# Performance work log

Measured on AMD Instinct MI355X. Metric: run time of the kernel, lower is better.

Reference implementation:

```python
import jax, jax.numpy as jnp
import numpy as np

N_EXPERTS = 8
D_MODEL = 1024
D_FF = 4096
BATCH = 4
SEQ = 4096


def setup_inputs() -> dict:
    key = jax.random.key(0)
    k1, k2, k3, k4 = jax.random.split(key, 4)
    hidden_states = jax.random.normal(k1, (BATCH, SEQ, D_MODEL), dtype=jnp.float32)
    expert_indices = jax.random.randint(k2, (BATCH, SEQ), 0, N_EXPERTS, dtype=jnp.int64)
    # Expert MLP params, scaled like standard init
    W1 = jax.random.normal(k3, (N_EXPERTS, D_MODEL, D_FF), dtype=jnp.float32) / np.sqrt(D_MODEL)
    b1 = jnp.zeros((N_EXPERTS, D_FF), dtype=jnp.float32)
    W2 = jax.random.normal(k4, (N_EXPERTS, D_FF, D_MODEL), dtype=jnp.float32) / np.sqrt(D_FF)
    b2 = jnp.zeros((N_EXPERTS, D_MODEL), dtype=jnp.float32)
    return {"hidden_states": hidden_states, "expert_indices": expert_indices,
            "W1": W1, "b1": b1, "W2": W2, "b2": b2}


def reference(hidden_states, expert_indices, W1, b1, W2, b2):
    B, S, D = hidden_states.shape
    flat = hidden_states.reshape(B * S, D)          # [T, D]
    idx = expert_indices.reshape(-1)                 # [T]
    out = jnp.zeros_like(flat)
    # Fixed small loop over experts (structurally distinct weights).
    # jit-friendly: each expert runs over all tokens, output masked per token.
    for e in range(W1.shape[0]):
        h = jax.nn.gelu(flat @ W1[e] + b1[e])        # [T, F]
        y = h @ W2[e] + b2[e]                        # [T, D]
        out = out + jnp.where((idx == e)[:, None], y, jnp.float32(0.0))
    return out.reshape(B, S, D)
```

## Files before the change

kernel.cpp:

```cpp
#include <hip/hip_runtime.h>

#define T_TOK 16384
#define DMODEL 1024
#define DFF 4096
#define NEXP 8
#define BM 128
#define BN 128
#define BK 32
#define LDA 40
#define LDB 40
#define TPAD (T_TOK + NEXP * BM)

#define SEG8 256
#define TP256 (T_TOK + NEXP * SEG8)
#define BM2 256
#define BN2 128
#define BK3 32

typedef __bf16 bf16x8 __attribute__((ext_vector_type(8)));
typedef float f32x4 __attribute__((ext_vector_type(4)));

#define GLOAD16(gp, lp) __builtin_amdgcn_global_load_lds( \
    (const __attribute__((address_space(1))) void*)(gp), \
    (__attribute__((address_space(3))) void*)(lp), 16, 0, 0)

#define MFMA16(a, b, c) __builtin_amdgcn_mfma_f32_16x16x32_bf16(a, b, c, 0, 0, 0)

__device__ __forceinline__ float gelu_f(float x) {
  float u = 0.7978845608028654f * (x + 0.044715f * x * x * x);
  float e = __expf(2.0f * u);
  float th = 1.0f - 2.0f / (e + 1.0f);
  return 0.5f * x * (1.0f + th);
}

__global__ void k_init(int* counts, int* cursors, int* bucket, int n) {
  int i = blockIdx.x * blockDim.x + threadIdx.x;
  if (i < n) bucket[i] = -1;
  if (i < NEXP) { counts[i] = 0; cursors[i] = 0; }
}

__global__ void k_hist(const int* __restrict__ idx, int* counts) {
  int t = blockIdx.x * blockDim.x + threadIdx.x;
  int e = (t < T_TOK) ? idx[t] : -1;
#pragma unroll
  for (int ex = 0; ex < NEXP; ex++) {
    unsigned long long m = __ballot(e == ex);
    if (((threadIdx.x & 63) == 0) && m)
      atomicAdd(&counts[ex], __popcll(m));
  }
}

__global__ void k_scan(const int* __restrict__ counts, int* po, int seg) {
  if (threadIdx.x == 0 && blockIdx.x == 0) {
    int acc = 0;
    for (int e = 0; e < NEXP; e++) {
      po[e] = acc;
      acc += ((counts[e] + seg - 1) / seg) * seg;
    }
    po[NEXP] = acc;
  }
}

__global__ void k_scatter(const int* __restrict__ idx, const int* __restrict__ po,
                          int* cursors, int* bucket) {
  int t = blockIdx.x * blockDim.x + threadIdx.x;
  int lane = threadIdx.x & 63;
  int e = (t < T_TOK) ? idx[t] : -1;
#pragma unroll
  for (int ex = 0; ex < NEXP; ex++) {
    unsigned long long m = __ballot(e == ex);
    if (e == ex) {
      int lead = __ffsll((long long)m) - 1;
      unsigned long long before = m & ((lane == 0) ? 0ull : ((1ull << lane) - 1ull));
      int base = 0;
      if (lane == lead) base = atomicAdd(&cursors[ex], __popcll(m));
      base = __shfl(base, lead);
      bucket[po[ex] + base + __popcll(before)] = t;
    }
  }
}

__global__ __launch_bounds__(256) void k_gather(
    const float* __restrict__ X, const int* __restrict__ bucket,
    __bf16* __restrict__ Xg)
{
  const int r = blockIdx.x;
  const int t = bucket[r];
  const int c = threadIdx.x * 4;
  float4 v = {0.f, 0.f, 0.f, 0.f};
  if (t >= 0) v = *(const float4*)&X[(size_t)t * DMODEL + c];
  union { __bf16 h[4]; uint2 u; } cv;
  cv.h[0] = (__bf16)v.x; cv.h[1] = (__bf16)v.y;
  cv.h[2] = (__bf16)v.z; cv.h[3] = (__bf16)v.w;
  *(uint2*)&Xg[(size_t)r * DMODEL + c] = cv.u;
}

__global__ __launch_bounds__(256) void k_transpose(
    const float* __restrict__ W, __bf16* __restrict__ Wt, int K, int N)
{
  __shared__ float tile[64][65];
  const size_t msz = (size_t)K * N;
  const float* __restrict__ src = W + (size_t)blockIdx.z * msz;
  __bf16* __restrict__ dst = Wt + (size_t)blockIdx.z * msz;
  const int n0 = blockIdx.x * 64, k0 = blockIdx.y * 64;
  const int tc = threadIdx.x & 15, tr = threadIdx.x >> 4;
#pragma unroll
  for (int i = 0; i < 4; i++) {
    float4 v = *(const float4*)&src[(size_t)(k0 + tr + i * 16) * N + n0 + tc * 4];
    tile[tr + i * 16][tc * 4 + 0] = v.x;
    tile[tr + i * 16][tc * 4 + 1] = v.y;
    tile[tr + i * 16][tc * 4 + 2] = v.z;
    tile[tr + i * 16][tc * 4 + 3] = v.w;
  }
  __syncthreads();
#pragma unroll
  for (int i = 0; i < 4; i++) {
    const int n = tr + i * 16;
    union { __bf16 h[4]; uint2 u; } cv;
    cv.h[0] = (__bf16)tile[tc * 4 + 0][n];
    cv.h[1] = (__bf16)tile[tc * 4 + 1][n];
    cv.h[2] = (__bf16)tile[tc * 4 + 2][n];
    cv.h[3] = (__bf16)tile[tc * 4 + 3][n];
    *(uint2*)&dst[(size_t)(n0 + n) * K + k0 + tc * 4] = cv.u;
  }
}

template <int K, int NCT, int CPX, bool SCATTER>
__global__ __launch_bounds__(512, 4) void k_gemmdb(
    const __bf16* __restrict__ Ag, const __bf16* __restrict__ Wt,
    const float* __restrict__ bias, const int* __restrict__ bucket,
    const int* __restrict__ po, void* __restrict__ outp)
{
  __shared__ __align__(16) __bf16 As[2][BM2 * BK3];
  __shared__ __align__(16) __bf16 Bs[2][BN2 * BK3];
  __shared__ int toks[BM2];

  const int tid = threadIdx.x;
  const int b = (int)blockIdx.x;
  const int idx = b >> 3;
  const int col_t = (b & 7) * CPX + (idx % CPX);
  const int row_t = idx / CPX;
  const int row0 = row_t * BM2;
  if (row0 >= po[NEXP]) return;
  const int nb0 = col_t * BN2;

  int e = 0;
#pragma unroll
  for (int k = 1; k < NEXP; k++) e = (row0 >= po[k]) ? k : e;
  const __bf16* __restrict__ Bw = Wt + (size_t)e * (size_t)(NCT * BN2) * K;

  if constexpr (SCATTER) {
    if (tid < BM2) toks[tid] = bucket[row0 + tid];
  }

  const int wave = tid >> 6;
  const int lane = tid & 63;
  const int wm = (wave >> 1) * 64;
  const int wn = (wave & 1) * 64;
  const int lm = lane & 15;
  const int lq = lane >> 4;

  const int srow = tid >> 2;
  const int skq  = (tid & 3) ^ ((tid >> 2) & 3) ^ ((tid >> 4) & 3);
  const __bf16* __restrict__ Asrc = Ag + (size_t)(row0 + srow) * K + skq * 8;
  const __bf16* __restrict__ Bsrc = Bw + (size_t)(nb0 + srow) * K + skq * 8;

  f32x4 acc[4][4];
#pragma unroll
  for (int i = 0; i < 4; i++)
#pragma unroll
    for (int j = 0; j < 4; j++) acc[i][j] = (f32x4)0.0f;

  const int ph = lq ^ (lm & 3) ^ ((lm >> 2) & 3);

#define STAGE(S, KT)                                                   \
  {                                                                    \
    const size_t ko = (size_t)(KT) * BK3;                              \
    __bf16* Ab = &As[S][wave * 512];                                   \
    __bf16* Bb = &Bs[S][wave * 512];                                   \
    GLOAD16(Asrc + ko, Ab);                                            \
    GLOAD16(Asrc + ko + (size_t)128 * K, Ab + 4096);                   \
    GLOAD16(Bsrc + ko, Bb);                                            \
  }

#define COMPUTE(S)                                                     \
  {                                                                    \
    bf16x8 af[4], bfr[4];                                              \
    _Pragma("unroll")                                                  \
    for (int i = 0; i < 4; i++)                                        \
      af[i] = *(const bf16x8*)&As[S][(wm + i * 16 + lm) * BK3 + ph * 8]; \
    _Pragma("unroll")                                                  \
    for (int j = 0; j < 4; j++)                                        \
      bfr[j] = *(const bf16x8*)&Bs[S][(wn + j * 16 + lm) * BK3 + ph * 8]; \
    __builtin_amdgcn_s_setprio(1);                                     \
    _Pragma("unroll")                                                  \
    for (int i = 0; i < 4; i++)                                        \
      _Pragma("unroll")                                                \
      for (int j = 0; j < 4; j++)                                      \
        acc[i][j] = MFMA16(af[i], bfr[j], acc[i][j]);                  \
    __builtin_amdgcn_s_setprio(0);                                     \
  }

  constexpr int NT = K / BK3;

  STAGE(0, 0)
  __syncthreads();

  for (int kt = 0; kt < NT - 2; kt += 2) {
    STAGE(1, kt + 1)
    COMPUTE(0)
    __syncthreads();
    STAGE(0, kt + 2)
    COMPUTE(1)
    __syncthreads();
  }
  STAGE(1, NT - 1)
  COMPUTE(0)
  __syncthreads();
  COMPUTE(1)

#undef STAGE
#undef COMPUTE

  constexpr int N = NCT * BN2;
  const float* __restrict__ bv = bias + (size_t)e * N;
  if constexpr (!SCATTER) {
    __bf16* __restrict__ Hq = (__bf16*)outp;
#pragma unroll
    for (int j = 0; j < 4; j++) {
      const int col = nb0 + wn + j * 16 + lm;
      const float bb = bv[col];
#pragma unroll
      for (int i = 0; i < 4; i++) {
#pragma unroll
        for (int r = 0; r < 4; r++) {
          int row = row0 + wm + i * 16 + lq * 4 + r;
          Hq[(size_t)row * N + col] = (__bf16)gelu_f(acc[i][j][r] + bb);
        }
      }
    }
  } else {
    float* __restrict__ O = (float*)outp;
#pragma unroll
    for (int j = 0; j < 4; j++) {
      const int col = nb0 + wn + j * 16 + lm;
      const float bb = bv[col];
#pragma unroll
      for (int i = 0; i < 4; i++) {
#pragma unroll
        for (int r = 0; r < 4; r++) {
          const int t = toks[wm + i * 16 + lq * 4 + r];
          if (t >= 0) O[(size_t)t * DMODEL + col] = acc[i][j][r] + bb;
        }
      }
    }
  }
}

__global__ __launch_bounds__(256, 2) void k_gemm1b(
    const __bf16* __restrict__ Ag, const __bf16* __restrict__ Wt,
    const float* __restrict__ b1, const int* __restrict__ po,
    __bf16* __restrict__ H)
{
  __shared__ __align__(16) __bf16 As[BM * BK];
  __shared__ __align__(16) __bf16 Bs[BN * BK];
  const int tid = threadIdx.x;
  const int b = (int)blockIdx.x;
  const int slot = b >> 3;
  const int row_t = (b & 7) + ((slot >> 5) << 3);
  const int col_t = slot & 31;
  const int row0 = row_t * BM;
  if (row0 >= po[NEXP]) return;
  const int nb0 = col_t * BN;

  int e = 0;
#pragma unroll
  for (int k = 1; k < NEXP; k++) e = (row0 >= po[k]) ? k : e;
  const __bf16* __restrict__ B = Wt + (size_t)e * DFF * DMODEL;

  f32x4 acc[4][4];
#pragma unroll
  for (int i = 0; i < 4; i++)
#pragma unroll
    for (int j = 0; j < 4; j++) acc[i][j] = (f32x4)0.0f;

  const int wave = tid >> 6;
  const int lane = tid & 63;
  const int wm = (wave & 1) * 64;
  const int wn = (wave >> 1) * 64;
  const int lm = lane & 15;
  const int lq = lane >> 4;

  const int sr = wave * 32 + (lane >> 2);
  const int g  = (lane & 3) ^ ((lane >> 3) & 3);
  const __bf16* Aptr = Ag + (size_t)(row0 + sr) * DMODEL + g * 8;
  const __bf16* Bptr = B + (size_t)(nb0 + sr) * DMODEL + g * 8;
  __bf16* Al = &As[wave * 1024];
  __bf16* Bl = &Bs[wave * 1024];
  const int sA = (lm >> 1) & 3;

  for (int k0 = 0; k0 < DMODEL; k0 += BK) {
    GLOAD16(Aptr + k0, Al);
    GLOAD16(Aptr + k0 + 16 * DMODEL, Al + 512);
    GLOAD16(Bptr + k0, Bl);
    GLOAD16(Bptr + k0 + 16 * DMODEL, Bl + 512);
    __syncthreads();

    bf16x8 af[4], bfr[4];
#pragma unroll
    for (int i = 0; i < 4; i++)
      af[i] = *(const bf16x8*)&As[(wm + i * 16 + lm) * BK + (lq ^ sA) * 8];
#pragma unroll
    for (int j = 0; j < 4; j++)
      bfr[j] = *(const bf16x8*)&Bs[(wn + j * 16 + lm) * BK + (lq ^ sA) * 8];
#pragma unroll
    for (int i = 0; i < 4; i++)
#pragma unroll
      for (int j = 0; j < 4; j++)
        acc[i][j] = __builtin_amdgcn_mfma_f32_16x16x32_bf16(af[i], bfr[j], acc[i][j], 0, 0, 0);
    __syncthreads();
  }

  const float* __restrict__ b1e = b1 + e * DFF;
#pragma unroll
  for (int j = 0; j < 4; j++) {
    const int col = nb0 + wn + j * 16 + lm;
    const float bias = b1e[col];
#pragma unroll
    for (int i = 0; i < 4; i++) {
#pragma unroll
      for (int r = 0; r < 4; r++) {
        int row = row0 + wm + i * 16 + lq * 4 + r;
        H[(size_t)row * DFF + col] = (__bf16)gelu_f(acc[i][j][r] + bias);
      }
    }
  }
}

__global__ __launch_bounds__(256, 2) void k_gemm2b(
    const __bf16* __restrict__ H, const __bf16* __restrict__ Wt,
    const float* __restrict__ b2, const int* __restrict__ bucket,
    const int* __restrict__ po, float* __restrict__ out)
{
  __shared__ __align__(16) __bf16 As[BM * BK];
  __shared__ __align__(16) __bf16 Bs[BN * BK];
  __shared__ int toks[BM];
  const int tid = threadIdx.x;
  const int b = (int)blockIdx.x;
  const int slot = b >> 3;
  const int row_t = (b & 7) + ((slot >> 3) << 3);
  const int col_t = slot & 7;
  const int row0 = row_t * BM;
  if (row0 >= po[NEXP]) return;
  const int nb0 = col_t * BN;

  int e = 0;
#pragma unroll
  for (int k = 1; k < NEXP; k++) e = (row0 >= po[k]) ? k : e;
  const __bf16* __restrict__ B = Wt + (size_t)e * DMODEL * DFF;

  if (tid < BM) toks[tid] = bucket[row0 + tid];

  f32x4 acc[4][4];
#pragma unroll
  for (int i = 0; i < 4; i++)
#pragma unroll
    for (int j = 0; j < 4; j++) acc[i][j] = (f32x4)0.0f;

  const int wave = tid >> 6;
  const int lane = tid & 63;
  const int wm = (wave & 1) * 64;
  const int wn = (wave >> 1) * 64;
  const int lm = lane & 15;
  const int lq = lane >> 4;

  const int sr = wave * 32 + (lane >> 2);
  const int g  = (lane & 3) ^ ((lane >> 3) & 3);
  const __bf16* Aptr = H + (size_t)(row0 + sr) * DFF + g * 8;
  const __bf16* Bptr = B + (size_t)(nb0 + sr) * DFF + g * 8;
  __bf16* Al = &As[wave * 1024];
  __bf16* Bl = &Bs[wave * 1024];
  const int sA = (lm >> 1) & 3;

  for (int k0 = 0; k0 < DFF; k0 += BK) {
    GLOAD16(Aptr + k0, Al);
    GLOAD16(Aptr + k0 + 16 * DFF, Al + 512);
    GLOAD16(Bptr + k0, Bl);
    GLOAD16(Bptr + k0 + 16 * DFF, Bl + 512);
    __syncthreads();

    bf16x8 af[4], bfr[4];
#pragma unroll
    for (int i = 0; i < 4; i++)
      af[i] = *(const bf16x8*)&As[(wm + i * 16 + lm) * BK + (lq ^ sA) * 8];
#pragma unroll
    for (int j = 0; j < 4; j++)
      bfr[j] = *(const bf16x8*)&Bs[(wn + j * 16 + lm) * BK + (lq ^ sA) * 8];
#pragma unroll
    for (int i = 0; i < 4; i++)
#pragma unroll
      for (int j = 0; j < 4; j++)
        acc[i][j] = __builtin_amdgcn_mfma_f32_16x16x32_bf16(af[i], bfr[j], acc[i][j], 0, 0, 0);
    __syncthreads();
  }

  const float* __restrict__ b2e = b2 + e * DMODEL;
#pragma unroll
  for (int j = 0; j < 4; j++) {
    const int col = nb0 + wn + j * 16 + lm;
    const float bias = b2e[col];
#pragma unroll
    for (int i = 0; i < 4; i++) {
#pragma unroll
      for (int r = 0; r < 4; r++) {
        int t = toks[wm + i * 16 + lq * 4 + r];
        if (t >= 0) out[(size_t)t * DMODEL + col] = acc[i][j][r] + bias;
      }
    }
  }
}

__global__ __launch_bounds__(256, 2) void k_gemm1(
    const float* __restrict__ X, const float* __restrict__ W1,
    const float* __restrict__ b1, const int* __restrict__ bucket,
    const int* __restrict__ po, __bf16* __restrict__ H, int base_row)
{
  __shared__ __bf16 As[BM * LDA];
  __shared__ __bf16 Bs[BN * LDB];
  __shared__ int toks[BM];
  const int tid = threadIdx.x;
  const int total = po[NEXP];
  const int row0 = base_row + (int)blockIdx.x * BM;
  if (row0 >= total) return;
  const int nb0 = (int)blockIdx.y * BN;
  int e = 0;
#pragma unroll
  for (int k = 1; k < NEXP; k++) e = (row0 >= po[k]) ? k : e;
  const float* __restrict__ W = W1 + (size_t)e * DMODEL * DFF;
  if (tid < BM) toks[tid] = bucket[row0 + tid];
  __syncthreads();
  f32x4 acc[4][4];
#pragma unroll
  for (int i = 0; i < 4; i++)
#pragma unroll
    for (int j = 0; j < 4; j++) acc[i][j] = (f32x4)0.0f;
  const int wave = tid >> 6, lane = tid & 63;
  const int wm = (wave & 1) * 64, wn = (wave >> 1) * 64;
  const int lm = lane & 15, lq = lane >> 4;
  const int bn = tid & 127, bkh = (tid >> 7) * 16;
  for (int k0 = 0; k0 < DMODEL; k0 += BK) {
#pragma unroll
    for (int i = 0; i < 4; i++) {
      int idx = tid + i * 256;
      int row = idx >> 3, kq = idx & 7;
      int t = toks[row];
      float4 v = {0.f, 0.f, 0.f, 0.f};
      if (t >= 0) v = *(const float4*)(X + (size_t)t * DMODEL + k0 + kq * 4);
      union { __bf16 h[4]; uint2 u; } cv;
      cv.h[0] = (__bf16)v.x; cv.h[1] = (__bf16)v.y;
      cv.h[2] = (__bf16)v.z; cv.h[3] = (__bf16)v.w;
      *(uint2*)&As[row * LDA + kq * 4] = cv.u;
    }
    {
      const float* src = W + (size_t)(k0 + bkh) * DFF + nb0 + bn;
      bf16x8 b0, b1v;
#pragma unroll
      for (int kk = 0; kk < 8; kk++) b0[kk] = (__bf16)src[(size_t)kk * DFF];
#pragma unroll
      for (int kk = 0; kk < 8; kk++) b1v[kk] = (__bf16)src[(size_t)(kk + 8) * DFF];
      *(bf16x8*)&Bs[bn * LDB + bkh] = b0;
      *(bf16x8*)&Bs[bn * LDB + bkh + 8] = b1v;
    }
    __syncthreads();
    bf16x8 af[4], bfr[4];
#pragma unroll
    for (int i = 0; i < 4; i++)
      af[i] = *(const bf16x8*)&As[(wm + i * 16 + lm) * LDA + lq * 8];
#pragma unroll
    for (int j = 0; j < 4; j++)
      bfr[j] = *(const bf16x8*)&Bs[(wn + j * 16 + lm) * LDB + lq * 8];
#pragma unroll
    for (int i = 0; i < 4; i++)
#pragma unroll
      for (int j = 0; j < 4; j++)
        acc[i][j] = __builtin_amdgcn_mfma_f32_16x16x32_bf16(af[i], bfr[j], acc[i][j], 0, 0, 0);
    __syncthreads();
  }
  const float* __restrict__ b1e = b1 + e * DFF;
  const int hbase = (int)blockIdx.x * BM;
#pragma unroll
  for (int j = 0; j < 4; j++) {
    const int col = nb0 + wn + j * 16 + lm;
    const float bias = b1e[col];
#pragma unroll
    for (int i = 0; i < 4; i++)
#pragma unroll
      for (int r = 0; r < 4; r++) {
        int row = hbase + wm + i * 16 + lq * 4 + r;
        H[(size_t)row * DFF + col] = (__bf16)gelu_f(acc[i][j][r] + bias);
      }
  }
}

__global__ __launch_bounds__(256, 2) void k_gemm2(
    const __bf16* __restrict__ H, const float* __restrict__ W2,
    const float* __restrict__ b2, const int* __restrict__ bucket,
    const int* __restrict__ po, float* __restrict__ out, int base_row)
{
  __shared__ __bf16 As[BM * LDA];
  __shared__ __bf16 Bs[BN * LDB];
  __shared__ int toks[BM];
  const int tid = threadIdx.x;
  const int total = po[NEXP];
  const int row0 = base_row + (int)blockIdx.x * BM;
  if (row0 >= total) return;
  const int nb0 = (int)blockIdx.y * BN;
  int e = 0;
#pragma unroll
  for (int k = 1; k < NEXP; k++) e = (row0 >= po[k]) ? k : e;
  const float* __restrict__ W = W2 + (size_t)e * DFF * DMODEL;
  if (tid < BM) toks[tid] = bucket[row0 + tid];
  __syncthreads();
  f32x4 acc[4][4];
#pragma unroll
  for (int i = 0; i < 4; i++)
#pragma unroll
    for (int j = 0; j < 4; j++) acc[i][j] = (f32x4)0.0f;
  const int wave = tid >> 6, lane = tid & 63;
  const int wm = (wave & 1) * 64, wn = (wave >> 1) * 64;
  const int lm = lane & 15, lq = lane >> 4;
  const int bn = tid & 127, bkh = (tid >> 7) * 16;
  const int hbase = (int)blockIdx.x * BM;
  for (int k0 = 0; k0 < DFF; k0 += BK) {
#pragma unroll
    for (int i = 0; i < 2; i++) {
      int idx = tid + i * 256;
      int row = idx >> 2, kq = idx & 3;
      bf16x8 v = *(const bf16x8*)(H + (size_t)(hbase + row) * DFF + k0 + kq * 8);
      *(bf16x8*)&As[row * LDA + kq * 8] = v;
    }
    {
      const float* src = W + (size_t)(k0 + bkh) * DMODEL + nb0 + bn;
      bf16x8 b0, b1v;
#pragma unroll
      for (int kk = 0; kk < 8; kk++) b0[kk] = (__bf16)src[(size_t)kk * DMODEL];
#pragma unroll
      for (int kk = 0; kk < 8; kk++) b1v[kk] = (__bf16)src[(size_t)(kk + 8) * DMODEL];
      *(bf16x8*)&Bs[bn * LDB + bkh] = b0;
      *(bf16x8*)&Bs[bn * LDB + bkh + 8] = b1v;
    }
    __syncthreads();
    bf16x8 af[4], bfr[4];
#pragma unroll
    for (int i = 0; i < 4; i++)
      af[i] = *(const bf16x8*)&As[(wm + i * 16 + lm) * LDA + lq * 8];
#pragma unroll
    for (int j = 0; j < 4; j++)
      bfr[j] = *(const bf16x8*)&Bs[(wn + j * 16 + lm) * LDB + lq * 8];
#pragma unroll
    for (int i = 0; i < 4; i++)
#pragma unroll
      for (int j = 0; j < 4; j++)
        acc[i][j] = __builtin_amdgcn_mfma_f32_16x16x32_bf16(af[i], bfr[j], acc[i][j], 0, 0, 0);
    __syncthreads();
  }
  const float* __restrict__ b2e = b2 + e * DMODEL;
#pragma unroll
  for (int j = 0; j < 4; j++) {
    const int col = nb0 + wn + j * 16 + lm;
    const float bias = b2e[col];
#pragma unroll
    for (int i = 0; i < 4; i++)
#pragma unroll
      for (int r = 0; r < 4; r++) {
        int t = toks[wm + i * 16 + lq * 4 + r];
        if (t >= 0) out[(size_t)t * DMODEL + col] = acc[i][j][r] + bias;
      }
  }
}

__global__ __launch_bounds__(256) void k_fallback(
    const float* __restrict__ X, const int* __restrict__ idx,
    const float* __restrict__ W1, const float* __restrict__ b1,
    const float* __restrict__ W2, const float* __restrict__ b2,
    float* __restrict__ out)
{
  __shared__ float xs[DMODEL];
  __shared__ float hs[DFF];
  const int t = blockIdx.x;
  const int e = idx[t];
  const int tid = threadIdx.x;
  const float* w1 = W1 + (size_t)e * DMODEL * DFF;
  const float* w2 = W2 + (size_t)e * DFF * DMODEL;
  for (int i = tid; i < DMODEL; i += 256) xs[i] = X[(size_t)t * DMODEL + i];
  __syncthreads();
  for (int f = tid; f < DFF; f += 256) {
    float a = 0.f;
    for (int d = 0; d < DMODEL; d++) a += xs[d] * w1[(size_t)d * DFF + f];
    hs[f] = gelu_f(a + b1[e * DFF + f]);
  }
  __syncthreads();
  for (int d = tid; d < DMODEL; d += 256) {
    float a = 0.f;
    for (int f = 0; f < DFF; f++) a += hs[f] * w2[(size_t)f * DMODEL + d];
    out[(size_t)t * DMODEL + d] = a + b2[e * DMODEL + d];
  }
}

extern "C" void kernel_launch(void* const* d_in, const int* in_sizes, int n_in,
                              void* d_out, int out_size, void* d_ws, size_t ws_size,
                              hipStream_t stream) {
  const float* X  = (const float*)d_in[0];
  const int*   EI = (const int*)d_in[1];
  const float* W1 = (const float*)d_in[2];
  const float* b1 = (const float*)d_in[3];
  const float* W2 = (const float*)d_in[4];
  const float* b2 = (const float*)d_in[5];
  float* out = (float*)d_out;

  char* ws = (char*)d_ws;
  int* counts  = (int*)(ws + 0);
  int* cursors = (int*)(ws + 32);
  int* po      = (int*)(ws + 64);
  int* bucket  = (int*)(ws + 512);

  {
    const size_t XG_OFF2 = 512 + (size_t)TP256 * 4;
    const size_t WT_OFF2 = XG_OFF2 + (size_t)TP256 * DMODEL * 2;
    const size_t HF_OFF2 = WT_OFF2 + (size_t)NEXP * DMODEL * DFF * 2;
    const size_t NEED2   = HF_OFF2 + (size_t)TP256 * DFF * 2;
    if (ws_size >= NEED2) {
      __bf16* Xg = (__bf16*)(ws + XG_OFF2);
      __bf16* Wt = (__bf16*)(ws + WT_OFF2);
      __bf16* H  = (__bf16*)(ws + HF_OFF2);

      k_init<<<(TP256 + 255) / 256, 256, 0, stream>>>(counts, cursors, bucket, TP256);
      k_hist<<<(T_TOK + 255) / 256, 256, 0, stream>>>(EI, counts);
      k_scan<<<1, 64, 0, stream>>>(counts, po, SEG8);
      k_scatter<<<(T_TOK + 255) / 256, 256, 0, stream>>>(EI, po, cursors, bucket);
      k_gather<<<TP256, 256, 0, stream>>>(X, bucket, Xg);
      k_transpose<<<dim3(DFF / 64, DMODEL / 64, NEXP), 256, 0, stream>>>(W1, Wt, DMODEL, DFF);
      k_gemmdb<DMODEL, DFF / BN2, (DFF / BN2) / 8, false>
          <<<(TP256 / BM2) * (DFF / BN2), 512, 0, stream>>>(Xg, Wt, b1, bucket, po, (void*)H);
      k_transpose<<<dim3(DMODEL / 64, DFF / 64, NEXP), 256, 0, stream>>>(W2, Wt, DFF, DMODEL);
      k_gemmdb<DFF, DMODEL / BN2, (DMODEL / BN2) / 8, true>
          <<<(TP256 / BM2) * (DMODEL / BN2), 512, 0, stream>>>(H, Wt, b2, bucket, po, (void*)out);
      return;
    }
  }

  const int Tpad = TPAD;

  const size_t XG_OFF = 70144;
  const size_t XG_SZ  = (size_t)Tpad * DMODEL * 2;
  const size_t WT_OFF = XG_OFF + XG_SZ;
  const size_t WT_SZ  = (size_t)NEXP * DMODEL * DFF * 2;
  const size_t HF_OFF = WT_OFF + WT_SZ;
  const size_t H_SZ   = (size_t)Tpad * DFF * 2;
  const size_t NEED   = HF_OFF + H_SZ;

  if (ws_size >= NEED) {
    __bf16* Xg = (__bf16*)(ws + XG_OFF);
    __bf16* Wt = (__bf16*)(ws + WT_OFF);
    __bf16* H  = (__bf16*)(ws + HF_OFF);

    k_init<<<(Tpad + 255) / 256, 256, 0, stream>>>(counts, cursors, bucket, Tpad);
    k_hist<<<(T_TOK + 255) / 256, 256, 0, stream>>>(EI, counts);
    k_scan<<<1, 64, 0, stream>>>(counts, po, BM);
    k_scatter<<<(T_TOK + 255) / 256, 256, 0, stream>>>(EI, po, cursors, bucket);
    k_gather<<<Tpad, 256, 0, stream>>>(X, bucket, Xg);
    k_transpose<<<dim3(DFF / 64, DMODEL / 64, NEXP), 256, 0, stream>>>(W1, Wt, DMODEL, DFF);
    k_gemm1b<<<(Tpad / BM) * (DFF / BN), 256, 0, stream>>>(Xg, Wt, b1, po, H);
    k_transpose<<<dim3(DMODEL / 64, DFF / 64, NEXP), 256, 0, stream>>>(W2, Wt, DFF, DMODEL);
    k_gemm2b<<<(Tpad / BM) * (DMODEL / BN), 256, 0, stream>>>(H, Wt, b2, bucket, po, out);
    return;
  }

  const size_t H_OFF = 512 + (size_t)Tpad * 4;
  __bf16* H = (__bf16*)(ws + H_OFF);
  size_t avail = (ws_size > H_OFF) ? ws_size - H_OFF : 0;
  long long crll = (long long)(avail / ((size_t)DFF * 2));
  int CR = (crll > Tpad) ? Tpad : (int)crll;
  CR -= CR % BM;
  if (CR < BM) {
    k_fallback<<<T_TOK, 256, 0, stream>>>(X, EI, W1, b1, W2, b2, out);
    return;
  }
  k_init<<<(Tpad + 255) / 256, 256, 0, stream>>>(counts, cursors, bucket, Tpad);
  k_hist<<<(T_TOK + 255) / 256, 256, 0, stream>>>(EI, counts);
  k_scan<<<1, 64, 0, stream>>>(counts, po, BM);
  k_scatter<<<(T_TOK + 255) / 256, 256, 0, stream>>>(EI, po, cursors, bucket);
  int nchunks = (Tpad + CR - 1) / CR;
  for (int c = 0; c < nchunks; c++) {
    int base = c * CR;
    int rows = Tpad - base; if (rows > CR) rows = CR;
    int mt = rows / BM;
    k_gemm1<<<dim3(mt, DFF / BN), 256, 0, stream>>>(X, W1, b1, bucket, po, H, base);
    k_gemm2<<<dim3(mt, DMODEL / BN), 256, 0, stream>>>(H, W2, b2, bucket, po, out, base);
  }
}
```

Baseline: 1.010 ms.

## Switch grouped GEMM to 128x128 tiles with BK=64 and row-major block swizzle

Changes the expert GEMM tile from 256x128x32 with 512 threads to 128x128x64 with 256 threads. It uses an 8-way XOR LDS swizzle for the wider K slice and issues eight async global-to-LDS loads per stage. It also remaps block indices so groups of eight consecutive blocks cover different row tiles sharing a column tile, and pads expert segments to 128 instead of 256 to cut padding waste. The intent is less padded work, fewer barriers per K, and better L2 reuse of weights. In exchange there is less A/B reuse per tile, fewer waves per block, and the s_setprio hints are removed.

New measurement: 984.3 us. 1.03x faster.

```diff
diff --git a/kernel.cpp b/kernel.cpp
--- a/kernel.cpp
+++ b/kernel.cpp
@@ -13,9 +13,9 @@
 
 #define SEG8 256
 #define TP256 (T_TOK + NEXP * SEG8)
-#define BM2 256
+#define BM2 128
 #define BN2 128
-#define BK3 32
+#define BK2 64
 
 typedef __bf16 bf16x8 __attribute__((ext_vector_type(8)));
 typedef float f32x4 __attribute__((ext_vector_type(4)));
@@ -125,21 +125,21 @@
   }
 }
 
-template <int K, int NCT, int CPX, bool SCATTER>
-__global__ __launch_bounds__(512, 4) void k_gemmdb(
+template <int K, int NCT, bool SCATTER>
+__global__ __launch_bounds__(256, 2) void k_gemmdb(
     const __bf16* __restrict__ Ag, const __bf16* __restrict__ Wt,
     const float* __restrict__ bias, const int* __restrict__ bucket,
     const int* __restrict__ po, void* __restrict__ outp)
 {
-  __shared__ __align__(16) __bf16 As[2][BM2 * BK3];
-  __shared__ __align__(16) __bf16 Bs[2][BN2 * BK3];
+  __shared__ __align__(16) __bf16 As[2][BM2 * BK2];
+  __shared__ __align__(16) __bf16 Bs[2][BN2 * BK2];
   __shared__ int toks[BM2];
 
   const int tid = threadIdx.x;
   const int b = (int)blockIdx.x;
   const int idx = b >> 3;
-  const int col_t = (b & 7) * CPX + (idx % CPX);
-  const int row_t = idx / CPX;
+  const int row_t = (b & 7) + ((idx / NCT) << 3);
+  const int col_t = idx % NCT;
   const int row0 = row_t * BM2;
   if (row0 >= po[NEXP]) return;
   const int nb0 = col_t * BN2;
@@ -160,8 +160,8 @@
   const int lm = lane & 15;
   const int lq = lane >> 4;
 
-  const int srow = tid >> 2;
-  const int skq  = (tid & 3) ^ ((tid >> 2) & 3) ^ ((tid >> 4) & 3);
+  const int srow = tid >> 3;
+  const int skq  = (tid & 7) ^ ((tid >> 3) & 7);
   const __bf16* __restrict__ Asrc = Ag + (size_t)(row0 + srow) * K + skq * 8;
   const __bf16* __restrict__ Bsrc = Bw + (size_t)(nb0 + srow) * K + skq * 8;
 
@@ -171,37 +171,44 @@
 #pragma unroll
     for (int j = 0; j < 4; j++) acc[i][j] = (f32x4)0.0f;
 
-  const int ph = lq ^ (lm & 3) ^ ((lm >> 2) & 3);
-
-#define STAGE(S, KT)                                                   \
-  {                                                                    \
-    const size_t ko = (size_t)(KT) * BK3;                              \
-    __bf16* Ab = &As[S][wave * 512];                                   \
-    __bf16* Bb = &Bs[S][wave * 512];                                   \
-    GLOAD16(Asrc + ko, Ab);                                            \
-    GLOAD16(Asrc + ko + (size_t)128 * K, Ab + 4096);                   \
-    GLOAD16(Bsrc + ko, Bb);                                            \
-  }
-
-#define COMPUTE(S)                                                     \
-  {                                                                    \
-    bf16x8 af[4], bfr[4];                                              \
-    _Pragma("unroll")                                                  \
-    for (int i = 0; i < 4; i++)                                        \
-      af[i] = *(const bf16x8*)&As[S][(wm + i * 16 + lm) * BK3 + ph * 8]; \
-    _Pragma("unroll")                                                  \
-    for (int j = 0; j < 4; j++)                                        \
-      bfr[j] = *(const bf16x8*)&Bs[S][(wn + j * 16 + lm) * BK3 + ph * 8]; \
-    __builtin_amdgcn_s_setprio(1);                                     \
-    _Pragma("unroll")                                                  \
-    for (int i = 0; i < 4; i++)                                        \
-      _Pragma("unroll")                                                \
-      for (int j = 0; j < 4; j++)                                      \
-        acc[i][j] = MFMA16(af[i], bfr[j], acc[i][j]);                  \
-    __builtin_amdgcn_s_setprio(0);                                     \
-  }
-
-  constexpr int NT = K / BK3;
+  const int sA = lm & 7;
+
+#define STAGE(S, KT)                                                    \
+  {                                                                     \
+    const size_t ko = (size_t)(KT) * BK2;                               \
+    __bf16* Ab = &As[S][wave * 512];                                    \
+    __bf16* Bb = &Bs[S][wave * 512];                                    \
+    GLOAD16(Asrc + ko,                   Ab);                           \
+    GLOAD16(Asrc + ko + (size_t)32 * K,  Ab + 2048);                    \
+    GLOAD16(Asrc + ko + (size_t)64 * K,  Ab + 4096);                    \
+    GLOAD16(Asrc + ko + (size_t)96 * K,  Ab + 6144);                    \
+    GLOAD16(Bsrc + ko,                   Bb);                           \
+    GLOAD16(Bsrc + ko + (size_t)32 * K,  Bb + 2048);                    \
+    GLOAD16(Bsrc + ko + (size_t)64 * K,  Bb + 4096);                    \
+    GLOAD16(Bsrc + ko + (size_t)96 * K,  Bb + 6144);                    \
+  }
+
+#define COMPUTE(S)                                                      \
+  {                                                                     \
+    _Pragma("unroll")                                                   \
+    for (int h = 0; h < 2; h++) {                                       \
+      const int ph = (h * 4 + lq) ^ sA;                                 \
+      bf16x8 af[4], bfr[4];                                             \
+      _Pragma("unroll")                                                 \
+      for (int i = 0; i < 4; i++)                                       \
+        af[i] = *(const bf16x8*)&As[S][(wm + i * 16 + lm) * BK2 + ph * 8]; \
+      _Pragma("unroll")                                                 \
+      for (int j = 0; j < 4; j++)                                       \
+        bfr[j] = *(const bf16x8*)&Bs[S][(wn + j * 16 + lm) * BK2 + ph * 8]; \
+      _Pragma("unroll")                                                 \
+      for (int i = 0; i < 4; i++)                                       \
+        _Pragma("unroll")                                               \
+        for (int j = 0; j < 4; j++)                                     \
+          acc[i][j] = MFMA16(af[i], bfr[j], acc[i][j]);                 \
+    }                                                                   \
+  }
+
+  constexpr int NT = K / BK2;
 
   STAGE(0, 0)
   __syncthreads();
@@ -636,15 +643,15 @@
 
       k_init<<<(TP256 + 255) / 256, 256, 0, stream>>>(counts, cursors, bucket, TP256);
       k_hist<<<(T_TOK + 255) / 256, 256, 0, stream>>>(EI, counts);
-      k_scan<<<1, 64, 0, stream>>>(counts, po, SEG8);
+      k_scan<<<1, 64, 0, stream>>>(counts, po, BM2);
       k_scatter<<<(T_TOK + 255) / 256, 256, 0, stream>>>(EI, po, cursors, bucket);
       k_gather<<<TP256, 256, 0, stream>>>(X, bucket, Xg);
       k_transpose<<<dim3(DFF / 64, DMODEL / 64, NEXP), 256, 0, stream>>>(W1, Wt, DMODEL, DFF);
-      k_gemmdb<DMODEL, DFF / BN2, (DFF / BN2) / 8, false>
-          <<<(TP256 / BM2) * (DFF / BN2), 512, 0, stream>>>(Xg, Wt, b1, bucket, po, (void*)H);
+      k_gemmdb<DMODEL, DFF / BN2, false>
+          <<<(TP256 / BM2) * (DFF / BN2), 256, 0, stream>>>(Xg, Wt, b1, bucket, po, (void*)H);
       k_transpose<<<dim3(DMODEL / 64, DFF / 64, NEXP), 256, 0, stream>>>(W2, Wt, DFF, DMODEL);
-      k_gemmdb<DFF, DMODEL / BN2, (DMODEL / BN2) / 8, true>
-          <<<(TP256 / BM2) * (DMODEL / BN2), 512, 0, stream>>>(H, Wt, b2, bucket, po, (void*)out);
+      k_gemmdb<DFF, DMODEL / BN2, true>
+          <<<(TP256 / BM2) * (DMODEL / BN2), 256, 0, stream>>>(H, Wt, b2, bucket, po, (void*)out);
       return;
     }
   }
```
